# Optimization experiments

Hardware: AMD Instinct MI355X
Metric: run time of the kernel (lower is better)

The kernel has to match this reference:

```python
import jax, jax.numpy as jnp
import numpy as np

MARGIN = 1.0
N, D = 8192, 128
NUM_CLASSES = 1024


def setup_inputs() -> dict:
    key = jax.random.key(0)
    k1, k2, k3 = jax.random.split(key, 3)
    a = jax.random.normal(k1, (N, D), dtype=jnp.float32)
    b = jax.random.normal(k2, (N, D), dtype=jnp.float32)
    # L2-normalize embeddings (standard for metric learning; keeps exp() stable)
    a = a / jnp.linalg.norm(a, axis=1, keepdims=True)
    b = b / jnp.linalg.norm(b, axis=1, keepdims=True)
    labels = jax.random.randint(k3, (N,), 0, NUM_CLASSES, dtype=jnp.int64 if jax.config.jax_enable_x64 else jnp.int32)
    return {"a": a, "b": b, "labels": labels}


def reference(a, b, labels):
    # S[i, j] = a_i . b_j  -- full pairwise similarity, one GEMM
    S = a @ b.T  # [N, N]
    same = labels[:, None] == labels[None, :]  # [N, N]
    eye = jnp.eye(labels.shape[0], dtype=bool)
    pos_mask = same & ~eye          # ordered positive pairs (i != j, same label)
    neg_mask = ~same                # ordered negative pairs (labels differ)
    # V[i] = sum_k in neg(i) exp(margin + S[i, k])
    V = jnp.sum(jnp.where(neg_mask, jnp.exp(MARGIN + S), 0.0), axis=1)  # [N]
    # per positive pair (i, j): max(log(V_i + V_j) - S_ij, 0)^2
    hinge = jnp.maximum(jnp.log(V[:, None] + V[None, :]) - S, 0.0)
    comp = jnp.where(pos_mask, hinge * hinge, 0.0)
    num_pos = jnp.sum(pos_mask)
    loss = jnp.sum(comp) / (2.0 * num_pos.astype(S.dtype))
    return loss
```

## Files before the change

kernel.cpp:

```cpp
#include <hip/hip_runtime.h>

#define NN 8192
#define DD 128
#define MAXCLS 64
#define NCHUNK 8
#define NBLK 512
#define LOG2E 1.4426950408889634f
#define E1    2.718281828459045f

typedef __attribute__((ext_vector_type(8))) short bf16x8;
typedef __attribute__((ext_vector_type(4))) float f32x4;

#if __has_builtin(__builtin_amdgcn_exp2f)
#define EXP2F(x) __builtin_amdgcn_exp2f(x)
#else
#define EXP2F(x) exp2f(x)
#endif

__device__ __forceinline__ void load16_lds(const unsigned short* g, unsigned short* l) {
    __builtin_amdgcn_global_load_lds(
        (const __attribute__((address_space(1))) unsigned int*)g,
        (__attribute__((address_space(3))) unsigned int*)l,
        16, 0, 0);
}

__device__ __forceinline__ unsigned short f2bf(float x) {
    unsigned u = __float_as_uint(x);
    u = (u + 0x7FFFu + ((u >> 16) & 1u)) >> 16;
    return (unsigned short)u;
}

__device__ __forceinline__ void st_agent(float* p, float v) {
    __hip_atomic_store(p, v, __ATOMIC_RELAXED, __HIP_MEMORY_SCOPE_AGENT);
}
__device__ __forceinline__ void st_agent(int* p, int v) {
    __hip_atomic_store(p, v, __ATOMIC_RELAXED, __HIP_MEMORY_SCOPE_AGENT);
}
__device__ __forceinline__ void st_agent(unsigned long long* p, unsigned long long v) {
    __hip_atomic_store(p, v, __ATOMIC_RELAXED, __HIP_MEMORY_SCOPE_AGENT);
}

__device__ __forceinline__ int xcd_id() {
    return (int)(__builtin_amdgcn_s_getreg(20 | (0 << 6) | (31 << 11)) & 7u);
}

__device__ __forceinline__ void grid_sync(int* subcnt, int* root, unsigned int* gen,
                                          unsigned int* gate, unsigned int* done) {
    __syncthreads();
    if (threadIdx.x == 0) {
        unsigned int g = __hip_atomic_load(gen, __ATOMIC_RELAXED, __HIP_MEMORY_SCOPE_AGENT);
        int xcd = xcd_id();
        unsigned int prev = __hip_atomic_exchange(&gate[xcd * 16], g + 1u,
                                                  __ATOMIC_RELAXED, __HIP_MEMORY_SCOPE_AGENT);
        bool leader = (prev != g + 1u);
        int sub = blockIdx.x & 7;
        int v = __hip_atomic_fetch_add(&subcnt[sub * 16], 1,
                                       __ATOMIC_RELAXED, __HIP_MEMORY_SCOPE_AGENT);
        if (v == (NBLK / 8) - 1) {
            __hip_atomic_store(&subcnt[sub * 16], 0, __ATOMIC_RELAXED, __HIP_MEMORY_SCOPE_AGENT);
            int r = __hip_atomic_fetch_add(root, 1, __ATOMIC_RELAXED, __HIP_MEMORY_SCOPE_AGENT);
            if (r == 7) {
                __hip_atomic_store(root, 0, __ATOMIC_RELAXED, __HIP_MEMORY_SCOPE_AGENT);
                __hip_atomic_store(gen, g + 1u, __ATOMIC_RELEASE, __HIP_MEMORY_SCOPE_AGENT);
            }
        }
        long long t0 = clock64();
        while (__hip_atomic_load(gen, __ATOMIC_RELAXED, __HIP_MEMORY_SCOPE_AGENT) == g) {
            __builtin_amdgcn_s_sleep(2);
            if (clock64() - t0 > (1LL << 24)) break;
        }
        if (leader) {
            (void)__hip_atomic_load(gen, __ATOMIC_ACQUIRE, __HIP_MEMORY_SCOPE_AGENT);
            __hip_atomic_store(&done[xcd * 16], g + 1u, __ATOMIC_RELAXED, __HIP_MEMORY_SCOPE_AGENT);
        } else {
            long long t1 = clock64();
            while (__hip_atomic_load(&done[xcd * 16], __ATOMIC_RELAXED, __HIP_MEMORY_SCOPE_AGENT) != g + 1u) {
                __builtin_amdgcn_s_sleep(2);
                if (clock64() - t1 > (1LL << 24)) break;
            }
        }
    }
    __syncthreads();
}

__global__ __launch_bounds__(256, 2) void ml_fused_kernel(
    const float* __restrict__ a, const float* __restrict__ b,
    const int* __restrict__ labels,
    unsigned short* __restrict__ abf, unsigned short* __restrict__ bbf,
    int* __restrict__ cnt, int* __restrict__ list,
    float* __restrict__ Vp,
    float* __restrict__ classLoss, int* __restrict__ classCnt,
    float* __restrict__ out,
    int* subcnt, int* root, unsigned int* gen,
    unsigned int* gate, unsigned int* done, int* doneCnt)
{
    __shared__ unsigned short Bs[2][128 * DD];
    __shared__ float red[2][64];

    const int tid = threadIdx.x;
    const int bid = blockIdx.x;

#pragma unroll
    for (int it = 0; it < 4; it++) {
        int t = it * (NBLK * 256) + bid * 256 + tid;
        const float* src = a;
        unsigned short* dst = abf;
        int idx = t;
        float scale = LOG2E;
        if (t >= 262144) { src = b; dst = bbf; idx = t - 262144; scale = 1.0f; }
        float4 v = ((const float4*)src)[idx];
        ushort4 o;
        o.x = f2bf(v.x * scale); o.y = f2bf(v.y * scale);
        o.z = f2bf(v.z * scale); o.w = f2bf(v.w * scale);
        union { ushort4 v4; unsigned long long u; } cvt;
        cvt.v4 = o;
        st_agent(((unsigned long long*)dst) + idx, cvt.u);
        if (t < NN) {
            int c = labels[t];
            int p = atomicAdd(&cnt[c], 1);
            if (p < MAXCLS) st_agent(&list[c * MAXCLS + p], t);
        }
    }

    grid_sync(subcnt, root, gen, gate, done);

    {
        const int lane = tid & 63;
        const int wv   = tid >> 6;
        const int row0 = (bid >> 3) * 128;
        const int j0   = (bid & 7) * 1024;

        const int lr = lane >> 4;
        const int sp = lane & 15;
        const int m  = lane & 15;
        const int q  = lane >> 4;
        const int xr = m & 7;

#pragma unroll
        for (int i = 0; i < 8; i++) {
            int rb = wv * 32 + i * 4;
            int r  = rb + lr;
            int cc = sp ^ (r & 7);
            load16_lds(&abf[(size_t)(row0 + r) * DD + cc * 8], &Bs[0][rb * DD]);
        }
#pragma unroll
        for (int i = 0; i < 8; i++) {
            int rb = wv * 32 + i * 4;
            int r  = rb + lr;
            int cc = sp ^ (r & 7);
            load16_lds(&bbf[(size_t)(j0 + r) * DD + cc * 8], &Bs[1][rb * DD]);
        }
        __syncthreads();

        const int wi = (wv >> 1) * 64;
        const int wj = (wv & 1) * 64;

        bf16x8 afr[4][4];
#pragma unroll
        for (int ti = 0; ti < 4; ti++)
#pragma unroll
            for (int ks = 0; ks < 4; ks++) {
                int r   = wi + ti * 16 + m;
                int pos = (ks * 4 + q) ^ xr;
                afr[ti][ks] = *(const bf16x8*)(&Bs[0][r * DD + pos * 8]);
            }
        asm volatile("s_waitcnt lgkmcnt(0)" ::: "memory");
        __syncthreads();

#pragma unroll
        for (int i = 0; i < 8; i++) {
            int rb = wv * 32 + i * 4;
            int r  = rb + lr;
            int cc = sp ^ (r & 7);
            load16_lds(&bbf[(size_t)(j0 + 128 + r) * DD + cc * 8], &Bs[0][rb * DD]);
        }

        float rs[4][4];
#pragma unroll
        for (int ti = 0; ti < 4; ti++)
#pragma unroll
            for (int rg = 0; rg < 4; rg++) rs[ti][rg] = 0.f;

        const f32x4 zero = {0.f, 0.f, 0.f, 0.f};
        f32x4 acc[4][4];

#define COMPUTE_TILE(BUF)                                                              \
        {                                                                              \
            __builtin_amdgcn_s_setprio(1);                                             \
            _Pragma("unroll")                                                          \
            for (int ks = 0; ks < 4; ks++) {                                           \
                bf16x8 bfr[4];                                                         \
                _Pragma("unroll")                                                      \
                for (int tj = 0; tj < 4; tj++) {                                       \
                    int r   = wj + tj * 16 + m;                                        \
                    int pos = (ks * 4 + q) ^ xr;                                       \
                    bfr[tj] = *(const bf16x8*)(&Bs[BUF][r * DD + pos * 8]);            \
                }                                                                      \
                _Pragma("unroll")                                                      \
                for (int ti = 0; ti < 4; ti++)                                         \
                    _Pragma("unroll")                                                  \
                    for (int tj = 0; tj < 4; tj++)                                     \
                        acc[ti][tj] = __builtin_amdgcn_mfma_f32_16x16x32_bf16(         \
                            afr[ti][ks], bfr[tj], (ks == 0) ? zero : acc[ti][tj],      \
                            0, 0, 0);                                                  \
            }                                                                          \
            __builtin_amdgcn_s_setprio(0);                                             \
        }

#define STAGE_B(JT, BUF)                                                               \
        _Pragma("unroll")                                                              \
        for (int i = 0; i < 8; i++) {                                                  \
            int rb = wv * 32 + i * 4;                                                  \
            int r  = rb + lr;                                                          \
            int cc = sp ^ (r & 7);                                                     \
            load16_lds(&bbf[(size_t)(j0 + (JT) * 128 + r) * DD + cc * 8],              \
                       &Bs[BUF][rb * DD]);                                             \
        }

#define EPILOGUE()                                                                     \
        _Pragma("unroll")                                                              \
        for (int ti = 0; ti < 4; ti++)                                                 \
            _Pragma("unroll")                                                          \
            for (int tj = 0; tj < 4; tj++) {                                           \
                f32x4 c = acc[ti][tj];                                                 \
                rs[ti][0] += EXP2F(c[0]);                                              \
                rs[ti][1] += EXP2F(c[1]);                                              \
                rs[ti][2] += EXP2F(c[2]);                                              \
                rs[ti][3] += EXP2F(c[3]);                                              \
            }

#pragma unroll 2
        for (int jt = 0; jt < 6; jt++) {
            const int cb = (jt + 1) & 1;
            COMPUTE_TILE(cb);
            asm volatile("s_waitcnt lgkmcnt(0)" ::: "memory");
            __builtin_amdgcn_s_barrier();
            STAGE_B(jt + 2, cb);
            EPILOGUE();
            asm volatile("s_waitcnt vmcnt(8)" ::: "memory");
            __builtin_amdgcn_s_barrier();
        }
        {
            COMPUTE_TILE(1);
            EPILOGUE();
            asm volatile("s_waitcnt vmcnt(0)" ::: "memory");
            __builtin_amdgcn_s_barrier();
        }
        {
            COMPUTE_TILE(0);
            EPILOGUE();
        }

#undef COMPUTE_TILE
#undef STAGE_B
#undef EPILOGUE

#pragma unroll
        for (int ti = 0; ti < 4; ti++)
#pragma unroll
            for (int rg = 0; rg < 4; rg++) {
                float v = rs[ti][rg];
                v += __shfl_xor(v, 1);
                v += __shfl_xor(v, 2);
                v += __shfl_xor(v, 4);
                v += __shfl_xor(v, 8);
                rs[ti][rg] = v;
            }

        if ((wv & 1) == 1 && m == 0) {
#pragma unroll
            for (int ti = 0; ti < 4; ti++)
#pragma unroll
                for (int rg = 0; rg < 4; rg++)
                    red[wv >> 1][ti * 16 + q * 4 + rg] = rs[ti][rg];
        }
        __syncthreads();
        if ((wv & 1) == 0 && m == 0) {
#pragma unroll
            for (int ti = 0; ti < 4; ti++)
#pragma unroll
                for (int rg = 0; rg < 4; rg++) {
                    int rloc = ti * 16 + q * 4 + rg;
                    st_agent(&Vp[(size_t)(bid & 7) * NN + row0 + wi + rloc],
                             rs[ti][rg] + red[wv >> 1][rloc]);
                }
        }
    }

    grid_sync(subcnt, root, gen, gate, done);

    {
        char* sm = (char*)&Bs[0][0];
        const int h  = tid >> 7;
        const int ht = tid & 127;
        int*   mem    = (int*)  (sm + h * 18432);
        float* sumExp = (float*)(sm + h * 18432 + 256);
        float* Vadj   = (float*)(sm + h * 18432 + 512);
        float* Sc     = (float*)(sm + h * 18432 + 1024);
        float* ps     = (float*)(sm + h * 18432 + 17408);
        int*   cs     = (int*)  (sm + h * 18432 + 17424);

        const int c = bid * 2 + h;
        int mc = cnt[c];
        if (mc > MAXCLS) mc = MAXCLS;

        float vsum = 0.f;
        if (ht < mc) {
            int r = list[c * MAXCLS + ht];
            mem[ht] = r;
#pragma unroll
            for (int jc = 0; jc < NCHUNK; jc++) vsum += Vp[(size_t)jc * NN + r];
        }
        if (ht < MAXCLS) sumExp[ht] = 0.f;
        __syncthreads();

        const int g = ht >> 4;
        const int l = ht & 15;
        const int tot1 = mc * mc;
        for (int pp = g; pp < tot1; pp += 8) {
            int i = pp / mc;
            int j = pp - i * mc;
            int ri = mem[i], rj = mem[j];
            const float4* ar = (const float4*)(a + (size_t)ri * DD) + l * 2;
            const float4* br = (const float4*)(b + (size_t)rj * DD) + l * 2;
            float4 a0 = ar[0], a1 = ar[1];
            float4 b0 = br[0], b1 = br[1];
            float s = 0.f;
            s = fmaf(a0.x, b0.x, s); s = fmaf(a0.y, b0.y, s);
            s = fmaf(a0.z, b0.z, s); s = fmaf(a0.w, b0.w, s);
            s = fmaf(a1.x, b1.x, s); s = fmaf(a1.y, b1.y, s);
            s = fmaf(a1.z, b1.z, s); s = fmaf(a1.w, b1.w, s);
            s += __shfl_xor(s, 1);
            s += __shfl_xor(s, 2);
            s += __shfl_xor(s, 4);
            s += __shfl_xor(s, 8);
            if (l == 0) {
                Sc[i * MAXCLS + j] = s;
                atomicAdd(&sumExp[i], __expf(s));
            }
        }
        __syncthreads();

        if (ht < mc) Vadj[ht] = E1 * (vsum - sumExp[ht]);
        __syncthreads();

        float partial = 0.f;
        int   count   = 0;
        for (int pp = ht; pp < tot1; pp += 128) {
            int i = pp / mc;
            int j = pp - i * mc;
            if (i != j) {
                float hg = fmaxf(logf(Vadj[i] + Vadj[j]) - Sc[i * MAXCLS + j], 0.f);
                partial += hg * hg;
                count++;
            }
        }
        for (int off = 32; off > 0; off >>= 1) {
            partial += __shfl_down(partial, off);
            count   += __shfl_down(count, off);
        }
        if ((ht & 63) == 0) { ps[ht >> 6] = partial; cs[ht >> 6] = count; }
        __syncthreads();
        if (ht == 0) {
            st_agent(&classLoss[c], ps[0] + ps[1]);
            st_agent(&classCnt[c],  cs[0] + cs[1]);
        }
    }

    __syncthreads();
    __shared__ int amLast;
    if (tid == 0) {
        int d = __hip_atomic_fetch_add(doneCnt, 1, __ATOMIC_RELAXED, __HIP_MEMORY_SCOPE_AGENT);
        amLast = (d == NBLK - 1);
    }
    __syncthreads();
    if (amLast) {
        __shared__ double dred[4];
        __shared__ long long cred[4];
        const int lane = tid & 63, wvv = tid >> 6;
        double dls = 0.0;
        long long dct = 0;
        for (int k = tid; k < 1024; k += 256) {
            dls += (double)__hip_atomic_load(&classLoss[k], __ATOMIC_RELAXED, __HIP_MEMORY_SCOPE_AGENT);
            dct += (long long)__hip_atomic_load(&classCnt[k], __ATOMIC_RELAXED, __HIP_MEMORY_SCOPE_AGENT);
        }
        for (int off = 32; off > 0; off >>= 1) {
            dls += __shfl_down(dls, off);
            dct += __shfl_down(dct, off);
        }
        if (lane == 0) { dred[wvv] = dls; cred[wvv] = dct; }
        __syncthreads();
        if (tid == 0) {
            double ls = dred[0] + dred[1] + dred[2] + dred[3];
            long long np = cred[0] + cred[1] + cred[2] + cred[3];
            out[0] = (float)(ls / (2.0 * (double)np));
        }
    }
}

extern "C" void kernel_launch(void* const* d_in, const int* in_sizes, int n_in,
                              void* d_out, int out_size, void* d_ws, size_t ws_size,
                              hipStream_t stream)
{
    const float* a      = (const float*)d_in[0];
    const float* b      = (const float*)d_in[1];
    const int*   labels = (const int*)d_in[2];
    float* out = (float*)d_out;

    char* ws = (char*)d_ws;
    unsigned short* abf = (unsigned short*)ws;
    unsigned short* bbf = (unsigned short*)(ws + 2097152);
    char*     base2     = ws + 4194304;
    int*      cnt       = (int*)(base2);
    int*      subcnt    = (int*)(base2 + 4096);
    int*      root      = (int*)(base2 + 4608);
    unsigned int* gen   = (unsigned int*)(base2 + 4612);
    unsigned int* gate  = (unsigned int*)(base2 + 4672);
    unsigned int* done  = (unsigned int*)(base2 + 5184);
    int*      doneCnt   = (int*)(base2 + 5696);
    float*    classLoss = (float*)(base2 + 8192);
    int*      classCnt  = (int*)(base2 + 12288);
    int*      list      = (int*)(base2 + 16384);
    float*    Vp        = (float*)(base2 + 278528);

    (void)hipMemsetAsync(cnt, 0, 8192, stream);

    ml_fused_kernel<<<NBLK, 256, 0, stream>>>(
        a, b, labels, abf, bbf, cnt, list, Vp, classLoss, classCnt, out,
        subcnt, root, gen, gate, done, doneCnt);
}
```

Before: 121.2 us.

## Streamline grid barrier with pre-elected per-XCD relays and padded counters

Each XCD's relay block is now elected once at kernel start through a claim counter, replacing the per-barrier exchange on a gate word. Only the relay polls the global generation word; the other blocks on that XCD poll a per-XCD done flag. Counters are padded to 128-byte spacing, sleep intervals are shortened, and the final last-block detection reuses the hierarchical subcounter tree instead of one contended atomic. The aim is to cut barrier latency and atomic contention, at the cost of more polling traffic and reliance on the pre-launch memset to reset the claim and done words.

```diff
diff --git a/kernel.cpp b/kernel.cpp
--- a/kernel.cpp
+++ b/kernel.cpp
@@ -36,46 +36,47 @@
 __device__ __forceinline__ void st_agent(int* p, int v) {
     __hip_atomic_store(p, v, __ATOMIC_RELAXED, __HIP_MEMORY_SCOPE_AGENT);
 }
+__device__ __forceinline__ void st_agent(unsigned int* p, unsigned int v) {
+    __hip_atomic_store(p, v, __ATOMIC_RELAXED, __HIP_MEMORY_SCOPE_AGENT);
+}
 __device__ __forceinline__ void st_agent(unsigned long long* p, unsigned long long v) {
     __hip_atomic_store(p, v, __ATOMIC_RELAXED, __HIP_MEMORY_SCOPE_AGENT);
 }
+__device__ __forceinline__ unsigned int ld_agent(const unsigned int* p) {
+    return __hip_atomic_load(p, __ATOMIC_RELAXED, __HIP_MEMORY_SCOPE_AGENT);
+}
 
 __device__ __forceinline__ int xcd_id() {
     return (int)(__builtin_amdgcn_s_getreg(20 | (0 << 6) | (31 << 11)) & 7u);
 }
 
 __device__ __forceinline__ void grid_sync(int* subcnt, int* root, unsigned int* gen,
-                                          unsigned int* gate, unsigned int* done) {
+                                          unsigned int* doneg, int relay, int myxcd,
+                                          int sub) {
     __syncthreads();
     if (threadIdx.x == 0) {
-        unsigned int g = __hip_atomic_load(gen, __ATOMIC_RELAXED, __HIP_MEMORY_SCOPE_AGENT);
-        int xcd = xcd_id();
-        unsigned int prev = __hip_atomic_exchange(&gate[xcd * 16], g + 1u,
-                                                  __ATOMIC_RELAXED, __HIP_MEMORY_SCOPE_AGENT);
-        bool leader = (prev != g + 1u);
-        int sub = blockIdx.x & 7;
-        int v = __hip_atomic_fetch_add(&subcnt[sub * 16], 1,
+        unsigned int g = ld_agent(gen);
+        int v = __hip_atomic_fetch_add(&subcnt[sub * 32], 1,
                                        __ATOMIC_RELAXED, __HIP_MEMORY_SCOPE_AGENT);
         if (v == (NBLK / 8) - 1) {
-            __hip_atomic_store(&subcnt[sub * 16], 0, __ATOMIC_RELAXED, __HIP_MEMORY_SCOPE_AGENT);
+            __hip_atomic_store(&subcnt[sub * 32], 0, __ATOMIC_RELAXED, __HIP_MEMORY_SCOPE_AGENT);
             int r = __hip_atomic_fetch_add(root, 1, __ATOMIC_RELAXED, __HIP_MEMORY_SCOPE_AGENT);
             if (r == 7) {
                 __hip_atomic_store(root, 0, __ATOMIC_RELAXED, __HIP_MEMORY_SCOPE_AGENT);
-                __hip_atomic_store(gen, g + 1u, __ATOMIC_RELEASE, __HIP_MEMORY_SCOPE_AGENT);
-            }
-        }
-        long long t0 = clock64();
-        while (__hip_atomic_load(gen, __ATOMIC_RELAXED, __HIP_MEMORY_SCOPE_AGENT) == g) {
-            __builtin_amdgcn_s_sleep(2);
-            if (clock64() - t0 > (1LL << 24)) break;
-        }
-        if (leader) {
-            (void)__hip_atomic_load(gen, __ATOMIC_ACQUIRE, __HIP_MEMORY_SCOPE_AGENT);
-            __hip_atomic_store(&done[xcd * 16], g + 1u, __ATOMIC_RELAXED, __HIP_MEMORY_SCOPE_AGENT);
+                st_agent(gen, g + 1u);
+            }
+        }
+        if (relay) {
+            long long t0 = clock64();
+            while (ld_agent(gen) == g) {
+                __builtin_amdgcn_s_sleep(1);
+                if (clock64() - t0 > (1LL << 24)) break;
+            }
+            st_agent(&doneg[myxcd * 32], g + 1u);
         } else {
             long long t1 = clock64();
-            while (__hip_atomic_load(&done[xcd * 16], __ATOMIC_RELAXED, __HIP_MEMORY_SCOPE_AGENT) != g + 1u) {
-                __builtin_amdgcn_s_sleep(2);
+            while ((int)(ld_agent(&doneg[myxcd * 32]) - (g + 1u)) < 0) {
+                __builtin_amdgcn_s_sleep(1);
                 if (clock64() - t1 > (1LL << 24)) break;
             }
         }
@@ -92,13 +93,21 @@
     float* __restrict__ classLoss, int* __restrict__ classCnt,
     float* __restrict__ out,
     int* subcnt, int* root, unsigned int* gen,
-    unsigned int* gate, unsigned int* done, int* doneCnt)
+    int* claim, unsigned int* doneg)
 {
     __shared__ unsigned short Bs[2][128 * DD];
     __shared__ float red[2][64];
 
     const int tid = threadIdx.x;
     const int bid = blockIdx.x;
+    const int sub = bid & 7;
+
+    int relay = 0, myxcd = 0;
+    if (tid == 0) {
+        myxcd = xcd_id();
+        relay = (__hip_atomic_fetch_add(&claim[myxcd * 32], 1,
+                                        __ATOMIC_RELAXED, __HIP_MEMORY_SCOPE_AGENT) == 0);
+    }
 
 #pragma unroll
     for (int it = 0; it < 4; it++) {
@@ -122,7 +131,7 @@
         }
     }
 
-    grid_sync(subcnt, root, gen, gate, done);
+    grid_sync(subcnt, root, gen, doneg, relay, myxcd, sub);
 
     {
         const int lane = tid & 63;
@@ -287,7 +296,7 @@
         }
     }
 
-    grid_sync(subcnt, root, gen, gate, done);
+    grid_sync(subcnt, root, gen, doneg, relay, myxcd, sub);
 
     {
         char* sm = (char*)&Bs[0][0];
@@ -370,8 +379,15 @@
     __syncthreads();
     __shared__ int amLast;
     if (tid == 0) {
-        int d = __hip_atomic_fetch_add(doneCnt, 1, __ATOMIC_RELAXED, __HIP_MEMORY_SCOPE_AGENT);
-        amLast = (d == NBLK - 1);
+        int last = 0;
+        int v = __hip_atomic_fetch_add(&subcnt[sub * 32], 1,
+                                       __ATOMIC_RELAXED, __HIP_MEMORY_SCOPE_AGENT);
+        if (v == (NBLK / 8) - 1) {
+            __hip_atomic_store(&subcnt[sub * 32], 0, __ATOMIC_RELAXED, __HIP_MEMORY_SCOPE_AGENT);
+            int r = __hip_atomic_fetch_add(root, 1, __ATOMIC_RELAXED, __HIP_MEMORY_SCOPE_AGENT);
+            if (r == 7) { __hip_atomic_store(root, 0, __ATOMIC_RELAXED, __HIP_MEMORY_SCOPE_AGENT); last = 1; }
+        }
+        amLast = last;
     }
     __syncthreads();
     if (amLast) {
@@ -413,11 +429,10 @@
     char*     base2     = ws + 4194304;
     int*      cnt       = (int*)(base2);
     int*      subcnt    = (int*)(base2 + 4096);
-    int*      root      = (int*)(base2 + 4608);
-    unsigned int* gen   = (unsigned int*)(base2 + 4612);
-    unsigned int* gate  = (unsigned int*)(base2 + 4672);
-    unsigned int* done  = (unsigned int*)(base2 + 5184);
-    int*      doneCnt   = (int*)(base2 + 5696);
+    int*      root      = (int*)(base2 + 5120);
+    unsigned int* gen   = (unsigned int*)(base2 + 5248);
+    int*      claim     = (int*)(base2 + 5376);
+    unsigned int* doneg = (unsigned int*)(base2 + 6400);
     float*    classLoss = (float*)(base2 + 8192);
     int*      classCnt  = (int*)(base2 + 12288);
     int*      list      = (int*)(base2 + 16384);
@@ -427,5 +442,5 @@
 
     ml_fused_kernel<<<NBLK, 256, 0, stream>>>(
         a, b, labels, abf, bbf, cnt, list, Vp, classLoss, classCnt, out,
-        subcnt, root, gen, gate, done, doneCnt);
-}
+        subcnt, root, gen, claim, doneg);
+}
```

New measurement: 111.7 us. 1.09x faster.
